# Optimization experiments

Hardware: AMD Instinct MI355X
Metric: run time of the kernel (lower is better)

The kernel has to match this reference:

```python
import jax, jax.numpy as jnp
import numpy as np
from functools import partial

B, L, TAPS, NMODES = 64, 4096, 32, 2
LR_W = 1.0 / 2**6   # assumed fixed LMS step for w (MetaNone: updates = -lr * grad)
LR_F = 1.0 / 2**7   # assumed fixed LMS step for f
GRAD_MAX = 30.0     # grad_max[0]
EPS = 1e-9


def setup_inputs() -> dict:
    key = jax.random.key(0)
    ks = jax.random.split(key, 6)
    u_r = jax.random.normal(ks[0], (B, L, TAPS, NMODES), jnp.float32)
    u_i = jax.random.normal(ks[1], (B, L, TAPS, NMODES), jnp.float32)
    x_r = jax.random.normal(ks[2], (B, L, NMODES), jnp.float32)
    x_i = jax.random.normal(ks[3], (B, L, NMODES), jnp.float32)
    # gauss_init: gaussian window, normalized, tiled to [B, Nmodes, Nmodes, taps]
    y = jnp.exp(-jnp.linspace(-5.0, 5.0, TAPS) ** 2)
    y = y / jnp.sum(y)
    w0_r = jnp.broadcast_to(y, (B, NMODES, NMODES, TAPS)).astype(jnp.float32)
    w0_i = jnp.zeros((B, NMODES, NMODES, TAPS), jnp.float32)
    f0_r = jnp.ones((B, NMODES), jnp.float32)
    f0_i = jnp.zeros((B, NMODES), jnp.float32)
    return dict(u_r=u_r, u_i=u_i, x_r=x_r, x_i=x_i,
                w0_r=w0_r, w0_i=w0_i, f0_r=f0_r, f0_i=f0_i)


def _adf_step(carry, inp):
    w, f = carry                      # w: [B,Nm,Nm,T] c64, f: [B,Nm] c64
    u_t, x_t = inp                    # u_t: [B,T,Nm], x_t: [B,Nm]
    v = jnp.einsum('bijt,btj->bi', w, u_t)          # mimo output [B,Nm]
    k = v * f
    d = x_t                                          # train mode: truth symbol
    psi_hat = jnp.abs(f) / f
    e_w = d * psi_hat - v
    e_f = d - k
    # normalized gradients (ddlms => normalized_grad=True)
    u_energy = jnp.sum(jnp.abs(u_t) ** 2, axis=(1, 2)) + EPS   # [B]
    uc = jnp.conjugate(jnp.swapaxes(u_t, 1, 2))                # [B,Nm,T]
    gw = -(1.0 / u_energy)[:, None, None, None] * e_w[:, :, None, None] * uc[:, None, :, :]
    v_energy = jnp.sum(jnp.abs(v) ** 2, axis=1) + EPS          # [B]
    gf = -(1.0 / v_energy)[:, None] * e_f * jnp.conjugate(v)
    ag = jnp.abs(gf)
    safe = jnp.where(ag > GRAD_MAX, ag, 1.0)
    gf = jnp.where(ag > GRAD_MAX, gf / safe * GRAD_MAX, gf)
    # MetaNone/LMS update: theta += -lr * grad
    w = w - LR_W * gw
    f = f - LR_F * gf
    return (w, f), k


def reference(u_r, u_i, x_r, x_i, w0_r, w0_i, f0_r, f0_i):
    u = u_r + 1j * u_i                # [B,L,T,Nm] complex64
    x = x_r + 1j * x_i                # [B,L,Nm]
    w0 = w0_r + 1j * w0_i
    f0 = f0_r + 1j * f0_i
    u_seq = jnp.swapaxes(u, 0, 1)     # [L,B,T,Nm] time-major for scan
    x_seq = jnp.swapaxes(x, 0, 1)     # [L,B,Nm]
    (_, _), z = jax.lax.scan(_adf_step, (w0, f0), (u_seq, x_seq))
    z = jnp.swapaxes(z, 0, 1)         # [B,L,Nm] equalized symbols
    return jnp.stack([z.real, z.imag], axis=-1)  # [B,L,Nm,2] float view
```

## Files before the change

### kernel.cpp

```cpp
#include <hip/hip_runtime.h>

namespace {

constexpr int kB = 64;
constexpr int kL = 4096;
constexpr float kLrW = 1.0f / 64.0f;
constexpr float kLrF = 1.0f / 128.0f;
constexpr float kGradMax = 30.0f;
constexpr float kEps = 1e-9f;
constexpr int kPF = 8;
constexpr int kNC = kL / kPF;

#define DPP_ADD_F32(v, ctrl)                                                   \
    v += __int_as_float(__builtin_amdgcn_update_dpp(                           \
        0, __float_as_int(v), (ctrl), 0xF, 0xF, true))

__device__ __forceinline__ float rl(float v, int l) {
    return __int_as_float(__builtin_amdgcn_readlane(__float_as_int(v), l));
}
__device__ __forceinline__ float frcp(float x) { return __builtin_amdgcn_rcpf(x); }
__device__ __forceinline__ float frsq(float x) { return __builtin_amdgcn_rsqf(x); }

__global__ __launch_bounds__(64, 1) void adf_kernel(
    const float* __restrict__ u_r, const float* __restrict__ u_i,
    const float* __restrict__ x_r, const float* __restrict__ x_i,
    const float* __restrict__ w0r_g, const float* __restrict__ w0i_g,
    const float* __restrict__ f0r_g, const float* __restrict__ f0i_g,
    float* __restrict__ out)
{
    const int b = blockIdx.x;
    const int lane = threadIdx.x;
    const int half = lane >> 5;
    const int tap  = lane & 31;
    const bool lo  = (half == 0);

    const int wbase = b * 128 + half * 64 + tap;
    float wAr = w0r_g[wbase],      wAi = w0i_g[wbase];
    float wBr = w0r_g[wbase + 32], wBi = w0i_g[wbase + 32];

    float fr = f0r_g[b * 2 + half];
    float fi = f0i_g[b * 2 + half];
    const float invf0 = frsq(fmaf(fr, fr, fi * fi));
    float psr = fr * invf0, psm = -fi * invf0;

    const float2* __restrict__ ur2 = (const float2*)u_r + (size_t)b * kL * 32;
    const float2* __restrict__ ui2 = (const float2*)u_i + (size_t)b * kL * 32;
    const float2* __restrict__ xr2 = (const float2*)x_r + (size_t)b * kL;
    const float2* __restrict__ xi2 = (const float2*)x_i + (size_t)b * kL;
    float2* __restrict__ ob2 = (float2*)out + (size_t)b * kL * 2;

    float2 Au[kPF], Aq[kPF], AxR[kPF], AxI[kPF];
    float2 Bu[kPF], Bq[kPF], BxR[kPF], BxI[kPF];
    float suA[kPF], suB[kPF];
    float kR[kPF], kI[kPF];
    float sdpr = 0.0f, sdpi = 0.0f;

    auto loadChunk = [&](float2 (&u)[kPF], float2 (&q)[kPF],
                         float2 (&xR)[kPF], float2 (&xI)[kPF], int chunk) {
#pragma unroll
        for (int s = 0; s < kPF; ++s) {
            int t = chunk * kPF + s;
            t = t < kL ? t : kL - 1;
            u[s]  = ur2[(size_t)t * 32 + tap];
            q[s]  = ui2[(size_t)t * 32 + tap];
            xR[s] = xr2[t];
            xI[s] = xi2[t];
        }
        __builtin_amdgcn_sched_barrier(0);
    };

    auto calcSu = [&](float2 (&u)[kPF], float2 (&q)[kPF], float (&su)[kPF]) {
        float e[kPF];
#pragma unroll
        for (int s = 0; s < kPF; ++s) {
            float t0 = u[s].x * u[s].x;
            t0 = fmaf(u[s].y, u[s].y, t0);
            t0 = fmaf(q[s].x, q[s].x, t0);
            t0 = fmaf(q[s].y, q[s].y, t0);
            e[s] = t0;
        }
#pragma unroll
        for (int s = 0; s < kPF; ++s) { DPP_ADD_F32(e[s], 0x111); }
#pragma unroll
        for (int s = 0; s < kPF; ++s) { DPP_ADD_F32(e[s], 0x112); }
#pragma unroll
        for (int s = 0; s < kPF; ++s) { DPP_ADD_F32(e[s], 0x114); }
#pragma unroll
        for (int s = 0; s < kPF; ++s) { DPP_ADD_F32(e[s], 0x118); }
#pragma unroll
        for (int s = 0; s < kPF; ++s) { DPP_ADD_F32(e[s], 0x142); }
#pragma unroll
        for (int s = 0; s < kPF; ++s) su[s] = kLrW * frcp(rl(e[s], 31) + kEps);
    };

    auto body = [&](int s, float2 (&u)[kPF], float2 (&q)[kPF],
                    float2 (&xR)[kPF], float2 (&xI)[kPF], float (&su)[kPF],
                    bool first) {
        const float2 uc = u[s], qc = q[s];
        if (first) {
            const float dr0 = lo ? xR[0].x : xR[0].y;
            const float di0 = lo ? xI[0].x : xI[0].y;
            const float dpr = fmaf(dr0, psr, -di0 * psm);
            const float dpi = fmaf(dr0, psm,  di0 * psr);
            sdpr = su[0] * dpr;
            sdpi = su[0] * dpi;
        }

        float pr = wAr * uc.x;
        pr = fmaf(-wAi, qc.x, pr); pr = fmaf(wBr, uc.y, pr); pr = fmaf(-wBi, qc.y, pr);
        float pi = wAr * qc.x;
        pi = fmaf(wAi, uc.x, pi); pi = fmaf(wBr, qc.y, pi); pi = fmaf(wBi, uc.y, pi);
        DPP_ADD_F32(pr, 0x111); DPP_ADD_F32(pi, 0x111);
        DPP_ADD_F32(pr, 0x112); DPP_ADD_F32(pi, 0x112);
        DPP_ADD_F32(pr, 0x114); DPP_ADD_F32(pi, 0x114);
        DPP_ADD_F32(pr, 0x118); DPP_ADD_F32(pi, 0x118);
        DPP_ADD_F32(pr, 0x142); DPP_ADD_F32(pi, 0x142);
        const float v0r = rl(pr, 31), v1r = rl(pr, 63);
        const float v0i = rl(pi, 31), v1i = rl(pi, 63);
        const float vr = lo ? v0r : v1r;
        const float vi = lo ? v0i : v1i;

        const float sun = su[s];
        const float tr = fmaf(-sun, vr, sdpr);
        const float ti = fmaf(-sun, vi, sdpi);
        wAr = fmaf(tr, uc.x, fmaf(ti, qc.x, wAr));
        wAi = fmaf(ti, uc.x, fmaf(-tr, qc.x, wAi));
        wBr = fmaf(tr, uc.y, fmaf(ti, qc.y, wBr));
        wBi = fmaf(ti, uc.y, fmaf(-tr, qc.y, wBi));

        const float dr = lo ? xR[s].x : xR[s].y;
        const float di = lo ? xI[s].x : xI[s].y;
        const float kr = fmaf(vr, fr, -vi * fi);
        const float ki = fmaf(vr, fi,  vi * fr);
        kR[s] = kr; kI[s] = ki;
        const float efr = dr - kr, efi = di - ki;
        float ven = v0r * v0r;
        ven = fmaf(v0i, v0i, ven);
        ven = fmaf(v1r, v1r, ven);
        ven = fmaf(v1i, v1i, ven);
        const float nv = frcp(ven + kEps);
        float hr = efr * vr; hr = fmaf(efi, vi, hr);
        float hi = efi * vr; hi = fmaf(-efr, vi, hi);
        hr *= nv; hi *= nv;
        float mg = hr * hr; mg = fmaf(hi, hi, mg);
        const float sc = fminf(1.0f, kGradMax * frsq(mg));
        const float scl = kLrF * sc;
        fr = fmaf(scl, hr, fr);
        fi = fmaf(scl, hi, fi);
        const float invf = frsq(fmaf(fr, fr, fi * fi));
        psr = fr * invf; psm = -fi * invf;

        if (s + 1 < kPF) {
            const float dnr = lo ? xR[s + 1].x : xR[s + 1].y;
            const float dni = lo ? xI[s + 1].x : xI[s + 1].y;
            const float dpr = fmaf(dnr, psr, -dni * psm);
            const float dpi = fmaf(dnr, psm,  dni * psr);
            sdpr = su[s + 1] * dpr;
            sdpi = su[s + 1] * dpi;
        }
    };

    auto processChunk = [&](int tbase, float2 (&u)[kPF], float2 (&q)[kPF],
                            float2 (&xR)[kPF], float2 (&xI)[kPF], float (&su)[kPF]) {
#pragma unroll
        for (int s = 0; s < kPF; ++s)
            body(s, u, q, xR, xI, su, s == 0);
        if (tap == 0) {
#pragma unroll
            for (int s = 0; s < kPF; ++s)
                ob2[(size_t)(tbase + s) * 2 + half] = make_float2(kR[s], kI[s]);
        }
    };

    loadChunk(Au, Aq, AxR, AxI, 0);
    loadChunk(Bu, Bq, BxR, BxI, 1);
    calcSu(Au, Aq, suA);

    for (int c = 0; c < kNC; c += 2) {
        processChunk(c * kPF, Au, Aq, AxR, AxI, suA);
        loadChunk(Au, Aq, AxR, AxI, (c + 2 < kNC) ? c + 2 : kNC - 1);
        calcSu(Bu, Bq, suB);
        processChunk((c + 1) * kPF, Bu, Bq, BxR, BxI, suB);
        loadChunk(Bu, Bq, BxR, BxI, (c + 3 < kNC) ? c + 3 : kNC - 1);
        calcSu(Au, Aq, suA);
    }
}

}

extern "C" void kernel_launch(void* const* d_in, const int* in_sizes, int n_in,
                              void* d_out, int out_size, void* d_ws, size_t ws_size,
                              hipStream_t stream) {
    const float* u_r  = (const float*)d_in[0];
    const float* u_i  = (const float*)d_in[1];
    const float* x_r  = (const float*)d_in[2];
    const float* x_i  = (const float*)d_in[3];
    const float* w0_r = (const float*)d_in[4];
    const float* w0_i = (const float*)d_in[5];
    const float* f0_r = (const float*)d_in[6];
    const float* f0_i = (const float*)d_in[7];
    float* out = (float*)d_out;

    dim3 grid(kB);
    dim3 block(64);
    adf_kernel<<<grid, block, 0, stream>>>(u_r, u_i, x_r, x_i,
                                           w0_r, w0_i, f0_r, f0_i, out);
}
```

Baseline: 838.0 us.

## Stage inputs via async global-to-LDS loads and skew the dot product one step ahead

Replaces the register-held double-buffered chunk loads with `global_load_lds` transfers into a two-slot LDS ring, synchronised by hand-placed `s_waitcnt vmcnt` counts. The loop is also software-pipelined: the next time step's MIMO dot product and its DPP reduction are computed right after the weight update, before the current step's f/psi update. This shortens the serial per-step dependency chain and frees VGPRs. In exchange it relies on exact vmcnt accounting, which also counts the output stores, and on LDS read latency now sitting inside the loop.

```diff
diff --git a/kernel.cpp b/kernel.cpp
--- a/kernel.cpp
+++ b/kernel.cpp
@@ -21,6 +21,9 @@
 __device__ __forceinline__ float frcp(float x) { return __builtin_amdgcn_rcpf(x); }
 __device__ __forceinline__ float frsq(float x) { return __builtin_amdgcn_rsqf(x); }
 
+typedef const __attribute__((address_space(1))) float gfloat;
+typedef __attribute__((address_space(3))) float lfloat;
+
 __global__ __launch_bounds__(64, 1) void adf_kernel(
     const float* __restrict__ u_r, const float* __restrict__ u_i,
     const float* __restrict__ x_r, const float* __restrict__ x_i,
@@ -28,6 +31,10 @@
     const float* __restrict__ f0r_g, const float* __restrict__ f0i_g,
     float* __restrict__ out)
 {
+    __shared__ float lu[2][kPF][64];
+    __shared__ float lq[2][kPF][64];
+    __shared__ float lx[2][64];
+
     const int b = blockIdx.x;
     const int lane = threadIdx.x;
     const int half = lane >> 5;
@@ -43,146 +50,164 @@
     const float invf0 = frsq(fmaf(fr, fr, fi * fi));
     float psr = fr * invf0, psm = -fi * invf0;
 
-    const float2* __restrict__ ur2 = (const float2*)u_r + (size_t)b * kL * 32;
-    const float2* __restrict__ ui2 = (const float2*)u_i + (size_t)b * kL * 32;
-    const float2* __restrict__ xr2 = (const float2*)x_r + (size_t)b * kL;
-    const float2* __restrict__ xi2 = (const float2*)x_i + (size_t)b * kL;
+    gfloat* gu = (gfloat*)u_r + (size_t)b * kL * 64 + lane;
+    gfloat* gq = (gfloat*)u_i + (size_t)b * kL * 64 + lane;
+    const int xl = lane & 31;
+    gfloat* gx = (xl < 16)
+        ? ((gfloat*)x_r + (size_t)b * kL * 2 + xl)
+        : ((gfloat*)x_i + (size_t)b * kL * 2 + (xl - 16));
     float2* __restrict__ ob2 = (float2*)out + (size_t)b * kL * 2;
 
-    float2 Au[kPF], Aq[kPF], AxR[kPF], AxI[kPF];
-    float2 Bu[kPF], Bq[kPF], BxR[kPF], BxI[kPF];
-    float suA[kPF], suB[kPF];
-    float kR[kPF], kI[kPF];
-    float sdpr = 0.0f, sdpi = 0.0f;
-
-    auto loadChunk = [&](float2 (&u)[kPF], float2 (&q)[kPF],
-                         float2 (&xR)[kPF], float2 (&xI)[kPF], int chunk) {
+    auto stage = [&](int chunk) {
+        const int par = chunk & 1;
 #pragma unroll
         for (int s = 0; s < kPF; ++s) {
-            int t = chunk * kPF + s;
-            t = t < kL ? t : kL - 1;
-            u[s]  = ur2[(size_t)t * 32 + tap];
-            q[s]  = ui2[(size_t)t * 32 + tap];
-            xR[s] = xr2[t];
-            xI[s] = xi2[t];
-        }
-        __builtin_amdgcn_sched_barrier(0);
+            __builtin_amdgcn_global_load_lds(gu + (size_t)(chunk * kPF + s) * 64,
+                                             (lfloat*)&lu[par][s][0], 4, 0, 0);
+            __builtin_amdgcn_global_load_lds(gq + (size_t)(chunk * kPF + s) * 64,
+                                             (lfloat*)&lq[par][s][0], 4, 0, 0);
+        }
+        __builtin_amdgcn_global_load_lds(gx + chunk * 16,
+                                         (lfloat*)&lx[par][0], 4, 0, 0);
     };
 
-    auto calcSu = [&](float2 (&u)[kPF], float2 (&q)[kPF], float (&su)[kPF]) {
-        float e[kPF];
-#pragma unroll
-        for (int s = 0; s < kPF; ++s) {
-            float t0 = u[s].x * u[s].x;
-            t0 = fmaf(u[s].y, u[s].y, t0);
-            t0 = fmaf(q[s].x, q[s].x, t0);
-            t0 = fmaf(q[s].y, q[s].y, t0);
-            e[s] = t0;
-        }
-#pragma unroll
-        for (int s = 0; s < kPF; ++s) { DPP_ADD_F32(e[s], 0x111); }
-#pragma unroll
-        for (int s = 0; s < kPF; ++s) { DPP_ADD_F32(e[s], 0x112); }
-#pragma unroll
-        for (int s = 0; s < kPF; ++s) { DPP_ADD_F32(e[s], 0x114); }
-#pragma unroll
-        for (int s = 0; s < kPF; ++s) { DPP_ADD_F32(e[s], 0x118); }
-#pragma unroll
-        for (int s = 0; s < kPF; ++s) { DPP_ADD_F32(e[s], 0x142); }
-#pragma unroll
-        for (int s = 0; s < kPF; ++s) su[s] = kLrW * frcp(rl(e[s], 31) + kEps);
-    };
-
-    auto body = [&](int s, float2 (&u)[kPF], float2 (&q)[kPF],
-                    float2 (&xR)[kPF], float2 (&xI)[kPF], float (&su)[kPF],
-                    bool first) {
-        const float2 uc = u[s], qc = q[s];
-        if (first) {
-            const float dr0 = lo ? xR[0].x : xR[0].y;
-            const float di0 = lo ? xI[0].x : xI[0].y;
-            const float dpr = fmaf(dr0, psr, -di0 * psm);
-            const float dpi = fmaf(dr0, psm,  di0 * psr);
-            sdpr = su[0] * dpr;
-            sdpi = su[0] * dpi;
-        }
-
-        float pr = wAr * uc.x;
-        pr = fmaf(-wAi, qc.x, pr); pr = fmaf(wBr, uc.y, pr); pr = fmaf(-wBi, qc.y, pr);
-        float pi = wAr * qc.x;
-        pi = fmaf(wAi, uc.x, pi); pi = fmaf(wBr, qc.y, pi); pi = fmaf(wBi, uc.y, pi);
+    auto ldu = [&](int par, int s) { return *(const float2*)&lu[par][s][tap * 2]; };
+    auto ldq = [&](int par, int s) { return *(const float2*)&lq[par][s][tap * 2]; };
+
+    stage(0);
+    stage(1);
+    asm volatile("s_waitcnt vmcnt(17)" ::: "memory");
+
+    float2 cu = ldu(0, 0), cq = ldq(0, 0);
+    float2 nu = ldu(0, 1), nq = ldq(0, 1);
+
+    float prC, piC;
+    {
+        float pr = wAr * cu.x;
+        pr = fmaf(-wAi, cq.x, pr); pr = fmaf(wBr, cu.y, pr); pr = fmaf(-wBi, cq.y, pr);
+        float pi = wAr * cq.x;
+        pi = fmaf(wAi, cu.x, pi); pi = fmaf(wBr, cq.y, pi); pi = fmaf(wBi, cu.y, pi);
         DPP_ADD_F32(pr, 0x111); DPP_ADD_F32(pi, 0x111);
         DPP_ADD_F32(pr, 0x112); DPP_ADD_F32(pi, 0x112);
         DPP_ADD_F32(pr, 0x114); DPP_ADD_F32(pi, 0x114);
         DPP_ADD_F32(pr, 0x118); DPP_ADD_F32(pi, 0x118);
         DPP_ADD_F32(pr, 0x142); DPP_ADD_F32(pi, 0x142);
-        const float v0r = rl(pr, 31), v1r = rl(pr, 63);
-        const float v0i = rl(pi, 31), v1i = rl(pi, 63);
-        const float vr = lo ? v0r : v1r;
-        const float vi = lo ? v0i : v1i;
-
-        const float sun = su[s];
-        const float tr = fmaf(-sun, vr, sdpr);
-        const float ti = fmaf(-sun, vi, sdpi);
-        wAr = fmaf(tr, uc.x, fmaf(ti, qc.x, wAr));
-        wAi = fmaf(ti, uc.x, fmaf(-tr, qc.x, wAi));
-        wBr = fmaf(tr, uc.y, fmaf(ti, qc.y, wBr));
-        wBi = fmaf(ti, uc.y, fmaf(-tr, qc.y, wBi));
-
-        const float dr = lo ? xR[s].x : xR[s].y;
-        const float di = lo ? xI[s].x : xI[s].y;
-        const float kr = fmaf(vr, fr, -vi * fi);
-        const float ki = fmaf(vr, fi,  vi * fr);
-        kR[s] = kr; kI[s] = ki;
-        const float efr = dr - kr, efi = di - ki;
-        float ven = v0r * v0r;
-        ven = fmaf(v0i, v0i, ven);
-        ven = fmaf(v1r, v1r, ven);
-        ven = fmaf(v1i, v1i, ven);
-        const float nv = frcp(ven + kEps);
-        float hr = efr * vr; hr = fmaf(efi, vi, hr);
-        float hi = efi * vr; hi = fmaf(-efr, vi, hi);
-        hr *= nv; hi *= nv;
-        float mg = hr * hr; mg = fmaf(hi, hi, mg);
-        const float sc = fminf(1.0f, kGradMax * frsq(mg));
-        const float scl = kLrF * sc;
-        fr = fmaf(scl, hr, fr);
-        fi = fmaf(scl, hi, fi);
-        const float invf = frsq(fmaf(fr, fr, fi * fi));
-        psr = fr * invf; psm = -fi * invf;
-
-        if (s + 1 < kPF) {
-            const float dnr = lo ? xR[s + 1].x : xR[s + 1].y;
-            const float dni = lo ? xI[s + 1].x : xI[s + 1].y;
-            const float dpr = fmaf(dnr, psr, -dni * psm);
-            const float dpi = fmaf(dnr, psm,  dni * psr);
-            sdpr = su[s + 1] * dpr;
-            sdpi = su[s + 1] * dpi;
-        }
-    };
-
-    auto processChunk = [&](int tbase, float2 (&u)[kPF], float2 (&q)[kPF],
-                            float2 (&xR)[kPF], float2 (&xI)[kPF], float (&su)[kPF]) {
-#pragma unroll
-        for (int s = 0; s < kPF; ++s)
-            body(s, u, q, xR, xI, su, s == 0);
+        prC = pr; piC = pi;
+    }
+
+    float sdpr = 0.f, sdpi = 0.f;
+    float kR[kPF], kI[kPF];
+
+    for (int c = 0; c < kNC; ++c) {
+        const int par = c & 1;
+        asm volatile("s_waitcnt vmcnt(25)" ::: "memory");
+
+        float su[kPF], dr[kPF], di[kPF];
+        {
+            float e[kPF];
+#pragma unroll
+            for (int s = 0; s < kPF; ++s) {
+                const float2 uu = ldu(par, s), qq = ldq(par, s);
+                float t0 = uu.x * uu.x;
+                t0 = fmaf(uu.y, uu.y, t0);
+                t0 = fmaf(qq.x, qq.x, t0);
+                t0 = fmaf(qq.y, qq.y, t0);
+                e[s] = t0;
+            }
+#pragma unroll
+            for (int s = 0; s < kPF; ++s) { DPP_ADD_F32(e[s], 0x111); }
+#pragma unroll
+            for (int s = 0; s < kPF; ++s) { DPP_ADD_F32(e[s], 0x112); }
+#pragma unroll
+            for (int s = 0; s < kPF; ++s) { DPP_ADD_F32(e[s], 0x114); }
+#pragma unroll
+            for (int s = 0; s < kPF; ++s) { DPP_ADD_F32(e[s], 0x118); }
+#pragma unroll
+            for (int s = 0; s < kPF; ++s) { DPP_ADD_F32(e[s], 0x142); }
+#pragma unroll
+            for (int s = 0; s < kPF; ++s)
+                su[s] = kLrW * frcp(rl(e[s], 31) + kEps);
+#pragma unroll
+            for (int s = 0; s < kPF; ++s) {
+                const float2 xr_ = *(const float2*)&lx[par][2 * s];
+                const float2 xi_ = *(const float2*)&lx[par][16 + 2 * s];
+                dr[s] = lo ? xr_.x : xr_.y;
+                di[s] = lo ? xi_.x : xi_.y;
+            }
+        }
+
+        {
+            const float dpr = fmaf(dr[0], psr, -di[0] * psm);
+            const float dpi = fmaf(dr[0], psm,  di[0] * psr);
+            sdpr = su[0] * dpr;
+            sdpi = su[0] * dpi;
+        }
+
+#pragma unroll
+        for (int s = 0; s < kPF; ++s) {
+            if (s == 6) asm volatile("s_waitcnt vmcnt(0)" ::: "memory");
+            const int s2 = (s + 2) & 7;
+            const int pb = (s + 2 >= kPF) ? (par ^ 1) : par;
+            const float2 fu = ldu(pb, s2), fq = ldq(pb, s2);
+
+            const float v0r = rl(prC, 31), v1r = rl(prC, 63);
+            const float v0i = rl(piC, 31), v1i = rl(piC, 63);
+            const float vr = lo ? v0r : v1r;
+            const float vi = lo ? v0i : v1i;
+
+            const float tr = fmaf(-su[s], vr, sdpr);
+            const float ti = fmaf(-su[s], vi, sdpi);
+            wAr = fmaf(tr, cu.x, fmaf(ti, cq.x, wAr));
+            wAi = fmaf(ti, cu.x, fmaf(-tr, cq.x, wAi));
+            wBr = fmaf(tr, cu.y, fmaf(ti, cq.y, wBr));
+            wBi = fmaf(ti, cu.y, fmaf(-tr, cq.y, wBi));
+
+            float pr = wAr * nu.x;
+            pr = fmaf(-wAi, nq.x, pr); pr = fmaf(wBr, nu.y, pr); pr = fmaf(-wBi, nq.y, pr);
+            float pi = wAr * nq.x;
+            pi = fmaf(wAi, nu.x, pi); pi = fmaf(wBr, nq.y, pi); pi = fmaf(wBi, nu.y, pi);
+            DPP_ADD_F32(pr, 0x111); DPP_ADD_F32(pi, 0x111);
+            DPP_ADD_F32(pr, 0x112); DPP_ADD_F32(pi, 0x112);
+            DPP_ADD_F32(pr, 0x114); DPP_ADD_F32(pi, 0x114);
+            DPP_ADD_F32(pr, 0x118); DPP_ADD_F32(pi, 0x118);
+            DPP_ADD_F32(pr, 0x142); DPP_ADD_F32(pi, 0x142);
+
+            const float kr = fmaf(vr, fr, -vi * fi);
+            const float ki = fmaf(vr, fi,  vi * fr);
+            kR[s] = kr; kI[s] = ki;
+            const float efr = dr[s] - kr, efi = di[s] - ki;
+            float ven = v0r * v0r;
+            ven = fmaf(v0i, v0i, ven);
+            ven = fmaf(v1r, v1r, ven);
+            ven = fmaf(v1i, v1i, ven);
+            const float nv = frcp(ven + kEps);
+            float hr = efr * vr; hr = fmaf(efi, vi, hr);
+            float hi = efi * vr; hi = fmaf(-efr, vi, hi);
+            hr *= nv; hi *= nv;
+            float mg = hr * hr; mg = fmaf(hi, hi, mg);
+            const float sc = fminf(1.0f, kGradMax * frsq(mg));
+            const float scl = kLrF * sc;
+            fr = fmaf(scl, hr, fr);
+            fi = fmaf(scl, hi, fi);
+            const float invf = frsq(fmaf(fr, fr, fi * fi));
+            psr = fr * invf; psm = -fi * invf;
+            if (s + 1 < kPF) {
+                const float dpr = fmaf(dr[s + 1], psr, -di[s + 1] * psm);
+                const float dpi = fmaf(dr[s + 1], psm,  di[s + 1] * psr);
+                sdpr = su[s + 1] * dpr;
+                sdpi = su[s + 1] * dpi;
+            }
+
+            prC = pr; piC = pi;
+            cu = nu; cq = nq; nu = fu; nq = fq;
+        }
+
         if (tap == 0) {
 #pragma unroll
             for (int s = 0; s < kPF; ++s)
-                ob2[(size_t)(tbase + s) * 2 + half] = make_float2(kR[s], kI[s]);
-        }
-    };
-
-    loadChunk(Au, Aq, AxR, AxI, 0);
-    loadChunk(Bu, Bq, BxR, BxI, 1);
-    calcSu(Au, Aq, suA);
-
-    for (int c = 0; c < kNC; c += 2) {
-        processChunk(c * kPF, Au, Aq, AxR, AxI, suA);
-        loadChunk(Au, Aq, AxR, AxI, (c + 2 < kNC) ? c + 2 : kNC - 1);
-        calcSu(Bu, Bq, suB);
-        processChunk((c + 1) * kPF, Bu, Bq, BxR, BxI, suB);
-        loadChunk(Bu, Bq, BxR, BxI, (c + 3 < kNC) ? c + 3 : kNC - 1);
-        calcSu(Au, Aq, suA);
+                ob2[(size_t)(c * kPF + s) * 2 + half] = make_float2(kR[s], kI[s]);
+        }
+        stage((c + 2 < kNC) ? c + 2 : kNC - 1);
     }
 }
 
```

Result: slower. 979.6 us (+16.9%).

## Precompute input energies in a parallel pre-pass and software-pipeline the LMS recurrence

Applied to the files above, without the earlier changes.

Adds a fully parallel pre-kernel that computes the per-step normalised step size from u energy and packs the truth symbols into a workspace, so these leave the serial recurrence. The main kernel streams u into LDS with asynchronous global_load_lds, and computes the next step's filter output right after the weight update so the reductions overlap with the f-update chain. It uses 16-lane DPP row sums plus permlane16/32 swaps in place of readlane-based reductions. The cost is an extra launch and workspace traffic, and a dependence on ws_size, with the old kernel kept as a fallback.

```diff
diff --git a/kernel.cpp b/kernel.cpp
--- a/kernel.cpp
+++ b/kernel.cpp
@@ -21,7 +21,218 @@
 __device__ __forceinline__ float frcp(float x) { return __builtin_amdgcn_rcpf(x); }
 __device__ __forceinline__ float frsq(float x) { return __builtin_amdgcn_rsqf(x); }
 
+__device__ __forceinline__ float rowsum16(float v) {
+    DPP_ADD_F32(v, 0x121);
+    DPP_ADD_F32(v, 0x122);
+    DPP_ADD_F32(v, 0x124);
+    DPP_ADD_F32(v, 0x128);
+    return v;
+}
+
+typedef unsigned u32x2v __attribute__((ext_vector_type(2)));
+
+__device__ __forceinline__ float pairsum16(float v) {
+#if __has_builtin(__builtin_amdgcn_permlane16_swap)
+    u32x2v r = __builtin_amdgcn_permlane16_swap(__float_as_uint(v),
+                                                __float_as_uint(v),
+                                                false, false);
+    return __uint_as_float(r[0]) + __uint_as_float(r[1]);
+#else
+    float a = v, b2;
+    asm("v_mov_b32 %1, %0\n\t"
+        "s_nop 1\n\t"
+        "v_permlane16_swap_b32 %0, %1"
+        : "+v"(a), "=&v"(b2));
+    return a + b2;
+#endif
+}
+
+__device__ __forceinline__ float pairsum32(float v) {
+#if __has_builtin(__builtin_amdgcn_permlane32_swap)
+    u32x2v r = __builtin_amdgcn_permlane32_swap(__float_as_uint(v),
+                                                __float_as_uint(v),
+                                                false, false);
+    return __uint_as_float(r[0]) + __uint_as_float(r[1]);
+#else
+    float a = v, b2;
+    asm("v_mov_b32 %1, %0\n\t"
+        "s_nop 1\n\t"
+        "v_permlane32_swap_b32 %0, %1"
+        : "+v"(a), "=&v"(b2));
+    return a + b2;
+#endif
+}
+
+typedef const __attribute__((address_space(1))) float gfloat;
+typedef __attribute__((address_space(3))) float lfloat;
+
+__global__ __launch_bounds__(256, 1) void pre_kernel(
+    const float* __restrict__ u_r, const float* __restrict__ u_i,
+    const float* __restrict__ x_r, const float* __restrict__ x_i,
+    float* __restrict__ su_ws, float4* __restrict__ xd_ws)
+{
+    const int lane = threadIdx.x & 63;
+    const int idx = blockIdx.x * 4 + (threadIdx.x >> 6);
+    const float a = u_r[(size_t)idx * 64 + lane];
+    const float c = u_i[(size_t)idx * 64 + lane];
+    float e = fmaf(a, a, c * c);
+    e = rowsum16(e);
+    e = pairsum16(e);
+    e = pairsum32(e);
+    if (lane == 0) {
+        su_ws[idx] = kLrW * frcp(e + kEps);
+        const float2 xr = *(const float2*)(x_r + (size_t)idx * 2);
+        const float2 xi = *(const float2*)(x_i + (size_t)idx * 2);
+        xd_ws[idx] = make_float4(xr.x, xr.y, xi.x, xi.y);
+    }
+}
+
 __global__ __launch_bounds__(64, 1) void adf_kernel(
+    const float* __restrict__ u_r, const float* __restrict__ u_i,
+    const float* __restrict__ w0r_g, const float* __restrict__ w0i_g,
+    const float* __restrict__ f0r_g, const float* __restrict__ f0i_g,
+    const float* __restrict__ su_p, const float4* __restrict__ xd_p,
+    float* __restrict__ out)
+{
+    __shared__ float lu[2][kPF][64];
+    __shared__ float lq[2][kPF][64];
+
+    const int b = blockIdx.x;
+    const int lane = threadIdx.x;
+    const int half = lane >> 5;
+    const int tap  = lane & 31;
+    const bool lo  = (half == 0);
+
+    const int wbase = b * 128 + half * 64 + tap;
+    float wAr = w0r_g[wbase],      wAi = w0i_g[wbase];
+    float wBr = w0r_g[wbase + 32], wBi = w0i_g[wbase + 32];
+
+    float fr = f0r_g[b * 2 + half];
+    float fi = f0i_g[b * 2 + half];
+    const float invf0 = frsq(fmaf(fr, fr, fi * fi));
+    float psr = fr * invf0, psm = -fi * invf0;
+
+    gfloat* gu = (gfloat*)u_r + (size_t)b * kL * 64 + lane;
+    gfloat* gq = (gfloat*)u_i + (size_t)b * kL * 64 + lane;
+    float2* __restrict__ ob2 = (float2*)out + (size_t)b * kL * 2;
+
+    auto stage = [&](int chunk) {
+        const int par = chunk & 1;
+#pragma unroll
+        for (int s = 0; s < kPF; ++s) {
+            __builtin_amdgcn_global_load_lds(gu + (size_t)(chunk * kPF + s) * 64,
+                                             (lfloat*)&lu[par][s][0], 4, 0, 0);
+            __builtin_amdgcn_global_load_lds(gq + (size_t)(chunk * kPF + s) * 64,
+                                             (lfloat*)&lq[par][s][0], 4, 0, 0);
+        }
+    };
+    auto ldu = [&](int par, int s) { return *(const float2*)&lu[par][s][tap * 2]; };
+    auto ldq = [&](int par, int s) { return *(const float2*)&lq[par][s][tap * 2]; };
+
+    stage(0);
+    stage(1);
+    asm volatile("s_waitcnt vmcnt(16)" ::: "memory");
+
+    float2 cu = ldu(0, 0), cq = ldq(0, 0);
+    float2 nu = ldu(0, 1), nq = ldq(0, 1);
+
+    float prC, piC;
+    {
+        float pr = wAr * cu.x;
+        pr = fmaf(-wAi, cq.x, pr); pr = fmaf(wBr, cu.y, pr); pr = fmaf(-wBi, cq.y, pr);
+        float pi = wAr * cq.x;
+        pi = fmaf(wAi, cu.x, pi); pi = fmaf(wBr, cq.y, pi); pi = fmaf(wBi, cu.y, pi);
+        pr = rowsum16(pr); pi = rowsum16(pi);
+        prC = pairsum16(pr); piC = pairsum16(pi);
+    }
+
+    float sdpr = 0.f, sdpi = 0.f;
+    float kR[kPF], kI[kPF];
+
+    for (int c = 0; c < kNC; ++c) {
+        const int par = c & 1;
+        const int base = b * kL + c * kPF;
+
+        float4 xq[kPF];
+        float suv[kPF];
+#pragma unroll
+        for (int s = 0; s < kPF; ++s) xq[s] = xd_p[base + s];
+#pragma unroll
+        for (int s = 0; s < kPF; ++s) suv[s] = su_p[base + s];
+
+        {
+            const float dr0 = lo ? xq[0].x : xq[0].y;
+            const float di0 = lo ? xq[0].z : xq[0].w;
+            sdpr = suv[0] * fmaf(dr0, psr, -di0 * psm);
+            sdpi = suv[0] * fmaf(dr0, psm,  di0 * psr);
+        }
+
+#pragma unroll
+        for (int s = 0; s < kPF; ++s) {
+            if (s == 6) asm volatile("s_waitcnt vmcnt(0)" ::: "memory");
+            const float2 fu = (s < 6) ? ldu(par, s + 2) : ldu(par ^ 1, s - 6);
+            const float2 fq = (s < 6) ? ldq(par, s + 2) : ldq(par ^ 1, s - 6);
+
+            const float vr = prC, vi = piC;
+
+            const float tr = fmaf(-suv[s], vr, sdpr);
+            const float ti = fmaf(-suv[s], vi, sdpi);
+            wAr = fmaf(tr, cu.x, fmaf(ti, cq.x, wAr));
+            wAi = fmaf(ti, cu.x, fmaf(-tr, cq.x, wAi));
+            wBr = fmaf(tr, cu.y, fmaf(ti, cq.y, wBr));
+            wBi = fmaf(ti, cu.y, fmaf(-tr, cq.y, wBi));
+
+            float pr = wAr * nu.x;
+            pr = fmaf(-wAi, nq.x, pr); pr = fmaf(wBr, nu.y, pr); pr = fmaf(-wBi, nq.y, pr);
+            float pi = wAr * nq.x;
+            pi = fmaf(wAi, nu.x, pi); pi = fmaf(wBr, nq.y, pi); pi = fmaf(wBi, nu.y, pi);
+            DPP_ADD_F32(pr, 0x121); DPP_ADD_F32(pi, 0x121);
+            DPP_ADD_F32(pr, 0x122); DPP_ADD_F32(pi, 0x122);
+            DPP_ADD_F32(pr, 0x124); DPP_ADD_F32(pi, 0x124);
+            DPP_ADD_F32(pr, 0x128); DPP_ADD_F32(pi, 0x128);
+            pr = pairsum16(pr);
+            pi = pairsum16(pi);
+
+            const float dr = lo ? xq[s].x : xq[s].y;
+            const float di = lo ? xq[s].z : xq[s].w;
+            const float kr = fmaf(vr, fr, -vi * fi);
+            const float ki = fmaf(vr, fi,  vi * fr);
+            kR[s] = kr; kI[s] = ki;
+            const float efr = dr - kr, efi = di - ki;
+            float mv2 = fmaf(vr, vr, vi * vi);
+            const float ven = pairsum32(mv2) + kEps;
+            const float nv = frcp(ven);
+            const float hr = fmaf(efi, vi, efr * vr) * nv;
+            const float hi = fmaf(-efr, vi, efi * vr) * nv;
+            const float mg = fmaf(hi, hi, hr * hr);
+            const float sc = fminf(1.0f, kGradMax * frsq(mg));
+            const float scl = kLrF * sc;
+            fr = fmaf(scl, hr, fr);
+            fi = fmaf(scl, hi, fi);
+            const float invf = frsq(fmaf(fr, fr, fi * fi));
+            psr = fr * invf; psm = -fi * invf;
+            if (s + 1 < kPF) {
+                const float dnr = lo ? xq[s + 1].x : xq[s + 1].y;
+                const float dni = lo ? xq[s + 1].z : xq[s + 1].w;
+                sdpr = suv[s + 1] * fmaf(dnr, psr, -dni * psm);
+                sdpi = suv[s + 1] * fmaf(dnr, psm,  dni * psr);
+            }
+
+            prC = pr; piC = pi;
+            cu = nu; cq = nq; nu = fu; nq = fq;
+        }
+
+        if (tap == 0) {
+#pragma unroll
+            for (int s = 0; s < kPF; ++s)
+                ob2[(size_t)(c * kPF + s) * 2 + half] = make_float2(kR[s], kI[s]);
+        }
+        asm volatile("s_waitcnt lgkmcnt(0)" ::: "memory");
+        stage((c + 2 < kNC) ? c + 2 : kNC - 1);
+    }
+}
+
+__global__ __launch_bounds__(64, 1) void adf_fb(
     const float* __restrict__ u_r, const float* __restrict__ u_i,
     const float* __restrict__ x_r, const float* __restrict__ x_i,
     const float* __restrict__ w0r_g, const float* __restrict__ w0i_g,
@@ -100,12 +311,9 @@
         if (first) {
             const float dr0 = lo ? xR[0].x : xR[0].y;
             const float di0 = lo ? xI[0].x : xI[0].y;
-            const float dpr = fmaf(dr0, psr, -di0 * psm);
-            const float dpi = fmaf(dr0, psm,  di0 * psr);
-            sdpr = su[0] * dpr;
-            sdpi = su[0] * dpi;
-        }
-
+            sdpr = su[0] * fmaf(dr0, psr, -di0 * psm);
+            sdpi = su[0] * fmaf(dr0, psm,  di0 * psr);
+        }
         float pr = wAr * uc.x;
         pr = fmaf(-wAi, qc.x, pr); pr = fmaf(wBr, uc.y, pr); pr = fmaf(-wBi, qc.y, pr);
         float pi = wAr * qc.x;
@@ -149,14 +357,11 @@
         fi = fmaf(scl, hi, fi);
         const float invf = frsq(fmaf(fr, fr, fi * fi));
         psr = fr * invf; psm = -fi * invf;
-
         if (s + 1 < kPF) {
             const float dnr = lo ? xR[s + 1].x : xR[s + 1].y;
             const float dni = lo ? xI[s + 1].x : xI[s + 1].y;
-            const float dpr = fmaf(dnr, psr, -dni * psm);
-            const float dpi = fmaf(dnr, psm,  dni * psr);
-            sdpr = su[s + 1] * dpr;
-            sdpi = su[s + 1] * dpi;
+            sdpr = su[s + 1] * fmaf(dnr, psr, -dni * psm);
+            sdpi = su[s + 1] * fmaf(dnr, psm,  dni * psr);
         }
     };
 
@@ -201,8 +406,16 @@
     const float* f0_i = (const float*)d_in[7];
     float* out = (float*)d_out;
 
-    dim3 grid(kB);
-    dim3 block(64);
-    adf_kernel<<<grid, block, 0, stream>>>(u_r, u_i, x_r, x_i,
-                                           w0_r, w0_i, f0_r, f0_i, out);
-}
+    const size_t need = (size_t)kB * kL * 20;
+    if (ws_size >= need) {
+        float* su_ws = (float*)d_ws;
+        float4* xd_ws = (float4*)((char*)d_ws + (size_t)kB * kL * 4);
+        dim3 pgrid(kB * kL / 4);
+        pre_kernel<<<pgrid, 256, 0, stream>>>(u_r, u_i, x_r, x_i, su_ws, xd_ws);
+        adf_kernel<<<dim3(kB), dim3(64), 0, stream>>>(
+            u_r, u_i, w0_r, w0_i, f0_r, f0_i, su_ws, xd_ws, out);
+    } else {
+        adf_fb<<<dim3(kB), dim3(64), 0, stream>>>(
+            u_r, u_i, x_r, x_i, w0_r, w0_i, f0_r, f0_i, out);
+    }
+}
```

Result: slower. 929.4 us (+10.9%).

## Precompute step sizes in parallel pre-kernel and use packed complex FMA

Applied to the files above, without the earlier changes.

Adds a fully parallel pre-kernel that computes the per-timestep normalized step size from the input energy and packs it with the target symbols into a workspace buffer. The serial scan kernel then loads these values instead of recomputing the energy reductions. It also rewrites the complex arithmetic with packed v_pk_fma inline assembly and folds the gradient clipping and normalization into a single fminf. The cost is an extra kernel launch and an extra round trip through the workspace. A fallback kernel is kept for when the workspace is too small.

```diff
diff --git a/kernel.cpp b/kernel.cpp
--- a/kernel.cpp
+++ b/kernel.cpp
@@ -21,7 +21,201 @@
 __device__ __forceinline__ float frcp(float x) { return __builtin_amdgcn_rcpf(x); }
 __device__ __forceinline__ float frsq(float x) { return __builtin_amdgcn_rsqf(x); }
 
+__device__ __forceinline__ void cfma(float2& a, const float2 s, const float2 u) {
+    asm("v_pk_fma_f32 %0, %1, %2, %0 op_sel:[1,1,0] op_sel_hi:[1,0,1] neg_lo:[0,1,0]\n\t"
+        "v_pk_fma_f32 %0, %1, %2, %0 op_sel:[0,0,0] op_sel_hi:[0,1,1]"
+        : "+v"(a) : "v"(s), "v"(u));
+}
+__device__ __forceinline__ void cfma_conj(float2& a, const float2 s, const float2 u) {
+    asm("v_pk_fma_f32 %0, %1, %2, %0 op_sel:[1,1,0] op_sel_hi:[1,0,1]\n\t"
+        "v_pk_fma_f32 %0, %1, %2, %0 op_sel:[0,0,0] op_sel_hi:[0,1,1] neg_hi:[0,1,0]"
+        : "+v"(a) : "v"(s), "v"(u));
+}
+__device__ __forceinline__ float2 cmul(const float2 s, const float2 u) {
+    float2 r;
+    asm("v_pk_mul_f32 %0, %1, %2 op_sel:[1,1] op_sel_hi:[1,0] neg_lo:[0,1]\n\t"
+        "v_pk_fma_f32 %0, %1, %2, %0 op_sel:[0,0,0] op_sel_hi:[0,1,1]"
+        : "=&v"(r) : "v"(s), "v"(u));
+    return r;
+}
+__device__ __forceinline__ float2 cmul_conj(const float2 s, const float2 u) {
+    float2 r;
+    asm("v_pk_mul_f32 %0, %1, %2 op_sel:[1,1] op_sel_hi:[1,0]\n\t"
+        "v_pk_fma_f32 %0, %1, %2, %0 op_sel:[0,0,0] op_sel_hi:[0,1,1] neg_hi:[0,1,0]"
+        : "=&v"(r) : "v"(s), "v"(u));
+    return r;
+}
+__device__ __forceinline__ float2 pk_fnma(const float2 s, const float2 u, const float2 c) {
+    float2 r;
+    asm("v_pk_fma_f32 %0, %1, %2, %3 neg_lo:[1,0,0] neg_hi:[1,0,0]"
+        : "=v"(r) : "v"(s), "v"(u), "v"(c));
+    return r;
+}
+__device__ __forceinline__ float2 pk_sub(const float2 a, const float2 b) {
+    float2 r;
+    asm("v_pk_add_f32 %0, %1, %2 neg_lo:[0,1] neg_hi:[0,1]" : "=v"(r) : "v"(a), "v"(b));
+    return r;
+}
+__device__ __forceinline__ float2 pk_mul(const float2 a, const float2 b) {
+    float2 r;
+    asm("v_pk_mul_f32 %0, %1, %2" : "=v"(r) : "v"(a), "v"(b));
+    return r;
+}
+
+typedef unsigned u32x2v __attribute__((ext_vector_type(2)));
+__device__ __forceinline__ float pairsum16(float v) {
+    u32x2v r = __builtin_amdgcn_permlane16_swap(__float_as_uint(v),
+                                                __float_as_uint(v), false, false);
+    return __uint_as_float(r[0]) + __uint_as_float(r[1]);
+}
+__device__ __forceinline__ float pairsum32(float v) {
+    u32x2v r = __builtin_amdgcn_permlane32_swap(__float_as_uint(v),
+                                                __float_as_uint(v), false, false);
+    return __uint_as_float(r[0]) + __uint_as_float(r[1]);
+}
+__device__ __forceinline__ float rowsum16(float v) {
+    DPP_ADD_F32(v, 0x121); DPP_ADD_F32(v, 0x122);
+    DPP_ADD_F32(v, 0x124); DPP_ADD_F32(v, 0x128);
+    return v;
+}
+
+__global__ __launch_bounds__(256, 1) void pre_kernel(
+    const float* __restrict__ u_r, const float* __restrict__ u_i,
+    const float* __restrict__ x_r, const float* __restrict__ x_i,
+    float* __restrict__ meta)
+{
+    const int lane = threadIdx.x & 63;
+    const int idx = blockIdx.x * 4 + (threadIdx.x >> 6);
+    const float a = u_r[(size_t)idx * 64 + lane];
+    const float c = u_i[(size_t)idx * 64 + lane];
+    float e = fmaf(a, a, c * c);
+    e = rowsum16(e);
+    e = pairsum16(e);
+    e = pairsum32(e);
+    if (lane == 0) {
+        const float su = kLrW * frcp(e + kEps);
+        const float2 xr = *(const float2*)(x_r + (size_t)idx * 2);
+        const float2 xi = *(const float2*)(x_i + (size_t)idx * 2);
+        float4* m = (float4*)(meta + (size_t)idx * 8);
+        m[0] = make_float4(su, su, xr.x, xi.x);
+        m[1] = make_float4(xr.y, xi.y, 0.0f, 0.0f);
+    }
+}
+
 __global__ __launch_bounds__(64, 1) void adf_kernel(
+    const float* __restrict__ u_r, const float* __restrict__ u_i,
+    const float* __restrict__ w0r_g, const float* __restrict__ w0i_g,
+    const float* __restrict__ f0r_g, const float* __restrict__ f0i_g,
+    const float* __restrict__ meta, float* __restrict__ out)
+{
+    const int b = blockIdx.x;
+    const int lane = threadIdx.x;
+    const int half = lane >> 5;
+    const int tap  = lane & 31;
+
+    const int wbase = b * 128 + half * 64 + tap;
+    float2 wA = make_float2(w0r_g[wbase],      w0i_g[wbase]);
+    float2 wB = make_float2(w0r_g[wbase + 32], w0i_g[wbase + 32]);
+
+    float2 f2 = make_float2(f0r_g[b * 2 + half], f0i_g[b * 2 + half]);
+    float2 psi2;
+    {
+        const float iv = frsq(fmaf(f2.x, f2.x, f2.y * f2.y));
+        psi2 = make_float2(f2.x * iv, -f2.y * iv);
+    }
+
+    const float2* __restrict__ ur2 = (const float2*)u_r + (size_t)b * kL * 32;
+    const float2* __restrict__ ui2 = (const float2*)u_i + (size_t)b * kL * 32;
+    const float* __restrict__ mp = meta + (size_t)b * kL * 8;
+    float2* __restrict__ ob2 = (float2*)out + (size_t)b * kL * 2;
+
+    float2 Au[kPF], Aq[kPF], Asu[kPF], Ad[kPF];
+    float2 Bu[kPF], Bq[kPF], Bsu[kPF], Bd[kPF];
+    float2 kO[kPF];
+    float2 sdp2 = make_float2(0.f, 0.f);
+
+    auto loadChunk = [&](float2 (&u)[kPF], float2 (&q)[kPF],
+                         float2 (&su)[kPF], float2 (&d)[kPF], int chunk) {
+#pragma unroll
+        for (int s = 0; s < kPF; ++s) {
+            int t = chunk * kPF + s;
+            t = t < kL ? t : kL - 1;
+            u[s]  = ur2[(size_t)t * 32 + tap];
+            q[s]  = ui2[(size_t)t * 32 + tap];
+            su[s] = *(const float2*)(mp + (size_t)t * 8);
+            d[s]  = *(const float2*)(mp + (size_t)t * 8 + 2 + 2 * half);
+        }
+        __builtin_amdgcn_sched_barrier(0);
+    };
+
+    auto body = [&](int s, float2 (&u)[kPF], float2 (&q)[kPF],
+                    float2 (&su)[kPF], float2 (&d)[kPF], bool first) {
+        const float2 cA = make_float2(u[s].x, q[s].x);
+        const float2 cB = make_float2(u[s].y, q[s].y);
+        if (first) {
+            sdp2 = pk_mul(su[0], cmul(d[0], psi2));
+        }
+        float2 p = cmul(wA, cA);
+        cfma(p, wB, cB);
+        float pr = p.x, pi = p.y;
+        DPP_ADD_F32(pr, 0x111); DPP_ADD_F32(pi, 0x111);
+        DPP_ADD_F32(pr, 0x112); DPP_ADD_F32(pi, 0x112);
+        DPP_ADD_F32(pr, 0x114); DPP_ADD_F32(pi, 0x114);
+        DPP_ADD_F32(pr, 0x118); DPP_ADD_F32(pi, 0x118);
+        DPP_ADD_F32(pr, 0x142); DPP_ADD_F32(pi, 0x142);
+        const float v0r = rl(pr, 31), v1r = rl(pr, 63);
+        const float v0i = rl(pi, 31), v1i = rl(pi, 63);
+        const float2 v2 = make_float2(half ? v1r : v0r, half ? v1i : v0i);
+
+        const float2 tau = pk_fnma(su[s], v2, sdp2);
+        cfma_conj(wA, tau, cA);
+        cfma_conj(wB, tau, cB);
+
+        const float2 k2 = cmul(v2, f2);
+        kO[s] = k2;
+        const float2 ef = pk_sub(d[s], k2);
+        float ven = v0r * v0r;
+        ven = fmaf(v0i, v0i, ven);
+        ven = fmaf(v1r, v1r, ven);
+        ven = fmaf(v1i, v1i, ven);
+        const float nv = frcp(ven + kEps);
+        const float2 H = cmul_conj(ef, v2);
+        const float MH = fmaf(H.x, H.x, H.y * H.y);
+        const float sc = fminf(nv, kGradMax * frsq(MH));
+        const float scl = kLrF * sc;
+        f2.x = fmaf(scl, H.x, f2.x);
+        f2.y = fmaf(scl, H.y, f2.y);
+        const float iff = frsq(fmaf(f2.x, f2.x, f2.y * f2.y));
+        psi2 = make_float2(f2.x * iff, -f2.y * iff);
+        if (s + 1 < kPF) {
+            sdp2 = pk_mul(su[s + 1], cmul(d[s + 1], psi2));
+        }
+    };
+
+    auto processChunk = [&](int tbase, float2 (&u)[kPF], float2 (&q)[kPF],
+                            float2 (&su)[kPF], float2 (&d)[kPF]) {
+#pragma unroll
+        for (int s = 0; s < kPF; ++s)
+            body(s, u, q, su, d, s == 0);
+        if (tap == 0) {
+#pragma unroll
+            for (int s = 0; s < kPF; ++s)
+                ob2[(size_t)(tbase + s) * 2 + half] = kO[s];
+        }
+    };
+
+    loadChunk(Au, Aq, Asu, Ad, 0);
+    loadChunk(Bu, Bq, Bsu, Bd, 1);
+
+    for (int c = 0; c < kNC; c += 2) {
+        processChunk(c * kPF, Au, Aq, Asu, Ad);
+        loadChunk(Au, Aq, Asu, Ad, (c + 2 < kNC) ? c + 2 : kNC - 1);
+        processChunk((c + 1) * kPF, Bu, Bq, Bsu, Bd);
+        loadChunk(Bu, Bq, Bsu, Bd, (c + 3 < kNC) ? c + 3 : kNC - 1);
+    }
+}
+
+__global__ __launch_bounds__(64, 1) void adf_fb(
     const float* __restrict__ u_r, const float* __restrict__ u_i,
     const float* __restrict__ x_r, const float* __restrict__ x_i,
     const float* __restrict__ w0r_g, const float* __restrict__ w0i_g,
@@ -100,12 +294,9 @@
         if (first) {
             const float dr0 = lo ? xR[0].x : xR[0].y;
             const float di0 = lo ? xI[0].x : xI[0].y;
-            const float dpr = fmaf(dr0, psr, -di0 * psm);
-            const float dpi = fmaf(dr0, psm,  di0 * psr);
-            sdpr = su[0] * dpr;
-            sdpi = su[0] * dpi;
-        }
-
+            sdpr = su[0] * fmaf(dr0, psr, -di0 * psm);
+            sdpi = su[0] * fmaf(dr0, psm,  di0 * psr);
+        }
         float pr = wAr * uc.x;
         pr = fmaf(-wAi, qc.x, pr); pr = fmaf(wBr, uc.y, pr); pr = fmaf(-wBi, qc.y, pr);
         float pi = wAr * qc.x;
@@ -149,14 +340,11 @@
         fi = fmaf(scl, hi, fi);
         const float invf = frsq(fmaf(fr, fr, fi * fi));
         psr = fr * invf; psm = -fi * invf;
-
         if (s + 1 < kPF) {
             const float dnr = lo ? xR[s + 1].x : xR[s + 1].y;
             const float dni = lo ? xI[s + 1].x : xI[s + 1].y;
-            const float dpr = fmaf(dnr, psr, -dni * psm);
-            const float dpi = fmaf(dnr, psm,  dni * psr);
-            sdpr = su[s + 1] * dpr;
-            sdpi = su[s + 1] * dpi;
+            sdpr = su[s + 1] * fmaf(dnr, psr, -dni * psm);
+            sdpi = su[s + 1] * fmaf(dnr, psm,  dni * psr);
         }
     };
 
@@ -201,8 +389,14 @@
     const float* f0_i = (const float*)d_in[7];
     float* out = (float*)d_out;
 
-    dim3 grid(kB);
-    dim3 block(64);
-    adf_kernel<<<grid, block, 0, stream>>>(u_r, u_i, x_r, x_i,
-                                           w0_r, w0_i, f0_r, f0_i, out);
-}
+    const size_t need = (size_t)kB * kL * 8 * sizeof(float);
+    if (ws_size >= need) {
+        float* meta = (float*)d_ws;
+        pre_kernel<<<dim3(kB * kL / 4), dim3(256), 0, stream>>>(u_r, u_i, x_r, x_i, meta);
+        adf_kernel<<<dim3(kB), dim3(64), 0, stream>>>(
+            u_r, u_i, w0_r, w0_i, f0_r, f0_i, meta, out);
+    } else {
+        adf_fb<<<dim3(kB), dim3(64), 0, stream>>>(
+            u_r, u_i, x_r, x_i, w0_r, w0_i, f0_r, f0_i, out);
+    }
+}
```

Measured after the change: 714.9 us. 14.7% less time.
